# Performance work log

Hardware: AMD Instinct MI355X
Metric: run time of the kernel (lower is better)

Reference implementation:

```python
import jax, jax.numpy as jnp
import numpy as np

N = 65536
E = 1048576
IN_DIM, HID, OUT = 500, 256, 64
ALPHA = 0.1
K = 10


def setup_inputs() -> dict:
    key = jax.random.key(0)
    ks = jax.random.split(key, 12)
    x = jax.random.normal(ks[0], (N, IN_DIM), dtype=jnp.float32)
    edge_row = jax.random.randint(ks[1], (E,), 0, N, dtype=jnp.int32)
    edge_col = jax.random.randint(ks[2], (E,), 0, N, dtype=jnp.int32)
    edge_weight = jax.random.uniform(ks[3], (E,), dtype=jnp.float32)
    # Linear params (Kaiming-uniform-like scale)
    def lin(k, fan_in, fan_out):
        kw, kb = jax.random.split(k)
        bound = 1.0 / np.sqrt(fan_in)
        W = jax.random.uniform(kw, (fan_in, fan_out), minval=-bound, maxval=bound, dtype=jnp.float32)
        b = jax.random.uniform(kb, (fan_out,), minval=-bound, maxval=bound, dtype=jnp.float32)
        return W, b
    W1, b1 = lin(ks[4], IN_DIM, HID)
    W2, b2 = lin(ks[5], HID, HID)
    W3, b3 = lin(ks[6], HID, OUT)
    return {"x": x, "W1": W1, "b1": b1, "W2": W2, "b2": b2,
            "W3": W3, "b3": b3, "edge_weight": edge_weight,
            "edge_row": edge_row, "edge_col": edge_col}


def reference(x, W1, b1, W2, b2, W3, b3, edge_weight, edge_row, edge_col):
    # MLP stack (dropout=0.0, norm_type='none')
    h = jax.nn.relu(x @ W1 + b1)          # [N, HID]
    h = jax.nn.relu(h @ W2 + b2)          # [N, HID]
    h = h @ W3 + b3                        # [N, OUT]
    h0 = h
    w = edge_weight[:, None]               # [E, 1]
    # APPNP: k steps of h = (1-alpha) * (A @ h) + alpha * h0 (SpMM via segment_sum)
    def step(h, _):
        msg = h[edge_col] * w               # [E, OUT] gather + scale
        agg = jax.ops.segment_sum(msg, edge_row, num_segments=N)  # [N, OUT]
        return (1.0 - ALPHA) * agg + ALPHA * h0, None
    h, _ = jax.lax.scan(step, h, None, length=K)
    return h
```

## Files before the change

kernel.cpp:

```cpp
#include <hip/hip_runtime.h>
#include <cstdint>
#include <cstddef>


#define N_NODES   65536
#define N_EDGES   1048576
#define IN_DIM    500
#define IN_PAD    512
#define HID_DIM   256
#define OUT_DIM   64
#define K_STEPS   10

#define NPW   8
#define CAPW  608
#define NCHUNK 16

typedef _Float16 half8 __attribute__((ext_vector_type(8)));
typedef float    f32x4 __attribute__((ext_vector_type(4)));

#define XB_OFF    0ULL
#define HA_OFF    0ULL
#define HB_OFF    33554432ULL
#define H1_OFF    67108864ULL
#define H0_OFF    67108864ULL
#define H2_OFF    100663296ULL
#define CNT2_OFF  100663296ULL
#define RANK_OFF  104857600ULL
#define TOT_OFF   109051904ULL
#define W1T_OFF   134217728ULL
#define W2T_OFF   134479872ULL
#define W3T_OFF   134610944ULL
#define ROWP_OFF  134643712ULL
#define EDG_OFF   135430400ULL

__device__ __forceinline__ void gload_lds16(const void* g, void* l) {
  __builtin_amdgcn_global_load_lds(
      (const __attribute__((address_space(1))) void*)g,
      (__attribute__((address_space(3))) void*)l, 16, 0, 0);
}

__device__ __forceinline__ float bf2f(unsigned short u) {
  return __uint_as_float(((unsigned)u) << 16);
}
__device__ __forceinline__ unsigned short f2bf_rne(float f) {
  unsigned u = __float_as_uint(f);
  u += 0x7fffu + ((u >> 16) & 1u);
  return (unsigned short)(u >> 16);
}
__device__ __forceinline__ float uaf(int u) {
  return __uint_as_float((unsigned)u);
}

template <int TM, int TN, int WM, int WN, bool RELU, int OMODE>
__global__ __launch_bounds__(256)
void gemm_kernel(const _Float16* __restrict__ A, const _Float16* __restrict__ B,
                 const float* __restrict__ bias, void* __restrict__ Cout,
                 int M, int Nn, int K) {
  static_assert((TM * 8) % 256 == 0 && (TN * 8) % 256 == 0, "tile");
  __shared__ uint4 As[TM * 8];
  __shared__ uint4 Bs[TN * 8];
  const int t    = threadIdx.x;
  const int lane = t & 63;
  const int wave = t >> 6;
  const int wm   = wave / WN;
  const int wn   = wave % WN;
  const int row0 = blockIdx.x * TM;
  const int col0 = blockIdx.y * TN;
  const int l15  = lane & 15;
  const int lq   = lane >> 4;

  f32x4 acc[4][4];
#pragma unroll
  for (int i = 0; i < 4; ++i)
#pragma unroll
    for (int j = 0; j < 4; ++j) acc[i][j] = (f32x4){0.f, 0.f, 0.f, 0.f};

  for (int k0 = 0; k0 < K; k0 += 64) {
#pragma unroll
    for (int i = 0; i < (TM * 8) / 256; ++i) {
      const int c = i * 256 + wave * 64 + lane;
      const int q = c / TM;
      const int r = c % TM;
      gload_lds16(A + (size_t)(row0 + r) * K + (k0 + q * 8),
                  As + i * 256 + wave * 64);
    }
#pragma unroll
    for (int i = 0; i < (TN * 8) / 256; ++i) {
      const int c = i * 256 + wave * 64 + lane;
      const int q = c / TN;
      const int r = c % TN;
      gload_lds16(B + (size_t)(col0 + r) * K + (k0 + q * 8),
                  Bs + i * 256 + wave * 64);
    }
    __syncthreads();
#pragma unroll
    for (int kk = 0; kk < 2; ++kk) {
      const int qa = kk * 4 + lq;
      half8 af[4], bfr[4];
#pragma unroll
      for (int mt = 0; mt < 4; ++mt)
        af[mt] = *((const half8*)(As + (qa * TM + wm * 64 + mt * 16 + l15)));
#pragma unroll
      for (int nt = 0; nt < 4; ++nt)
        bfr[nt] = *((const half8*)(Bs + (qa * TN + wn * 64 + nt * 16 + l15)));
#pragma unroll
      for (int mt = 0; mt < 4; ++mt)
#pragma unroll
        for (int nt = 0; nt < 4; ++nt)
          acc[mt][nt] = __builtin_amdgcn_mfma_f32_16x16x32_f16(
              af[mt], bfr[nt], acc[mt][nt], 0, 0, 0);
    }
    __syncthreads();
  }

#pragma unroll
  for (int mt = 0; mt < 4; ++mt) {
#pragma unroll
    for (int nt = 0; nt < 4; ++nt) {
      const int col = col0 + wn * 64 + nt * 16 + l15;
      const float bv = bias[col];
#pragma unroll
      for (int r = 0; r < 4; ++r) {
        const int row = row0 + wm * 64 + mt * 16 + lq * 4 + r;
        float v = acc[mt][nt][r] + bv;
        if (RELU) v = fmaxf(v, 0.f);
        if (OMODE == 0)
          ((_Float16*)Cout)[(size_t)row * Nn + col] = (_Float16)v;
        else if (OMODE == 1)
          ((unsigned short*)Cout)[(size_t)row * Nn + col] = f2bf_rne(v);
        else
          ((float*)Cout)[(size_t)row * Nn + col] = v;
      }
    }
  }
}

__global__ void cast_x_kernel(const float* __restrict__ x,
                              _Float16* __restrict__ xb) {
  const int c = blockIdx.x * blockDim.x + threadIdx.x;
  if (c >= N_NODES * (IN_PAD / 8)) return;
  const int row = c >> 6;
  const int c8  = (c & 63) << 3;
  half8 o;
  if (c8 + 8 <= IN_DIM) {
    const float4* p = (const float4*)(x + (size_t)row * IN_DIM + c8);
    const float4 a = p[0], b = p[1];
    o[0] = (_Float16)a.x; o[1] = (_Float16)a.y;
    o[2] = (_Float16)a.z; o[3] = (_Float16)a.w;
    o[4] = (_Float16)b.x; o[5] = (_Float16)b.y;
    o[6] = (_Float16)b.z; o[7] = (_Float16)b.w;
  } else {
#pragma unroll
    for (int j = 0; j < 8; ++j) {
      const float v = (c8 + j < IN_DIM) ? x[(size_t)row * IN_DIM + c8 + j] : 0.f;
      o[j] = (_Float16)v;
    }
  }
  *(half8*)(xb + (size_t)c * 8) = o;
}

__global__ void cast_w_kernel(const float* __restrict__ W,
                              _Float16* __restrict__ Wt, int K, int Kpad,
                              int Nn) {
  const int idx = blockIdx.x * blockDim.x + threadIdx.x;
  if (idx >= Nn * Kpad) return;
  const int n = idx / Kpad;
  const int k = idx % Kpad;
  const float v = (k < K) ? W[(size_t)k * Nn + n] : 0.f;
  Wt[idx] = (_Float16)v;
}

__global__ void hist2_kernel(const int* __restrict__ row,
                             int* __restrict__ cnt2, int* __restrict__ rank,
                             int E) {
  const int e = blockIdx.x * blockDim.x + threadIdx.x;
  if (e < E)
    rank[e] = atomicAdd(&cnt2[(e >> 16) * N_NODES + row[e]], 1);
}

__global__ void scan_tot_kernel(const int* __restrict__ cnt2,
                                int* __restrict__ tot) {
  const int r = blockIdx.x * blockDim.x + threadIdx.x;
  int s = 0;
#pragma unroll
  for (int c = 0; c < NCHUNK; ++c) s += cnt2[c * N_NODES + r];
  tot[r] = s;
}

__global__ void scan_kernel(const int4* __restrict__ counts4,
                            int* __restrict__ rowptr) {
  __shared__ int part[1024];
  const int t = threadIdx.x;
  const int base = t * 16;
  int4 c[16];
  int s = 0;
#pragma unroll
  for (int i = 0; i < 16; ++i) {
    c[i] = counts4[base + i];
    s += c[i].x + c[i].y + c[i].z + c[i].w;
  }
  part[t] = s;
  __syncthreads();
  for (int off = 1; off < 1024; off <<= 1) {
    const int v = (t >= off) ? part[t - off] : 0;
    __syncthreads();
    part[t] += v;
    __syncthreads();
  }
  int run = (t == 0) ? 0 : part[t - 1];
#pragma unroll
  for (int i = 0; i < 16; ++i) {
    int4 r;
    r.x = run; run += c[i].x;
    r.y = run; run += c[i].y;
    r.z = run; run += c[i].z;
    r.w = run; run += c[i].w;
    ((int4*)rowptr)[base + i] = r;
  }
  if (t == 1023) rowptr[N_NODES] = run;
}

__global__ void chunkbase_kernel(int* __restrict__ cnt2,
                                 const int* __restrict__ rowptr) {
  const int r = blockIdx.x * blockDim.x + threadIdx.x;
  int run = rowptr[r];
#pragma unroll
  for (int c = 0; c < NCHUNK; ++c) {
    const int t = cnt2[c * N_NODES + r];
    cnt2[c * N_NODES + r] = run;
    run += t;
  }
}

__global__ void scatter2_kernel(const int* __restrict__ row,
                                const int* __restrict__ col,
                                const float* __restrict__ w,
                                const int* __restrict__ rank,
                                const int* __restrict__ cbase,
                                int2* __restrict__ edges, int E) {
  const int e = blockIdx.x * blockDim.x + threadIdx.x;
  if (e < E) {
    const int pos = cbase[(e >> 16) * N_NODES + row[e]] + rank[e];
    edges[pos] = make_int2(col[e], __float_as_int(w[e]));
  }
}

template <bool OUT_F32>
__global__ __launch_bounds__(256)
void prop_step(const unsigned short* __restrict__ hin,
               const unsigned short* __restrict__ h0,
               void* __restrict__ hout, const int* __restrict__ rowptr,
               const int2* __restrict__ edges) {
  __shared__ int2 eb[4][CAPW];
  const int wave = threadIdx.x >> 6;
  const int lane = threadIdx.x & 63;
  const int node0 = (blockIdx.x * 4 + wave) * NPW;

  const int rp  = rowptr[node0 + min(lane, NPW)];
  const int beg = __shfl(rp, 0);
  const int nE  = __shfl(rp, NPW) - beg;
  const int rrel = rp - beg;
  int2* __restrict__ ebw = eb[wave];

  const bool fast = (nE <= CAPW);
  if (fast) {
    for (int i = lane; i < nE; i += 64) ebw[i] = edges[beg + i];
    __builtin_amdgcn_s_waitcnt(0);
  }

  for (int i = 0; i < NPW; ++i) {
    const int nb = __shfl(rrel, i);
    const int ne = __shfl(rrel, i + 1);
    float a0 = 0.f, a1 = 0.f, a2 = 0.f, a3 = 0.f;
    if (fast) {
      int j = nb;
      for (; j + 8 <= ne; j += 8) {
        const int2 e0 = ebw[j + 0];
        const int2 e1 = ebw[j + 1];
        const int2 e2 = ebw[j + 2];
        const int2 e3 = ebw[j + 3];
        const int2 e4 = ebw[j + 4];
        const int2 e5 = ebw[j + 5];
        const int2 e6 = ebw[j + 6];
        const int2 e7 = ebw[j + 7];
        const float v0 = bf2f(hin[((size_t)e0.x << 6) | lane]);
        const float v1 = bf2f(hin[((size_t)e1.x << 6) | lane]);
        const float v2 = bf2f(hin[((size_t)e2.x << 6) | lane]);
        const float v3 = bf2f(hin[((size_t)e3.x << 6) | lane]);
        const float v4 = bf2f(hin[((size_t)e4.x << 6) | lane]);
        const float v5 = bf2f(hin[((size_t)e5.x << 6) | lane]);
        const float v6 = bf2f(hin[((size_t)e6.x << 6) | lane]);
        const float v7 = bf2f(hin[((size_t)e7.x << 6) | lane]);
        a0 = fmaf(uaf(e0.y), v0, a0);
        a1 = fmaf(uaf(e1.y), v1, a1);
        a2 = fmaf(uaf(e2.y), v2, a2);
        a3 = fmaf(uaf(e3.y), v3, a3);
        a0 = fmaf(uaf(e4.y), v4, a0);
        a1 = fmaf(uaf(e5.y), v5, a1);
        a2 = fmaf(uaf(e6.y), v6, a2);
        a3 = fmaf(uaf(e7.y), v7, a3);
      }
      for (; j + 4 <= ne; j += 4) {
        const int2 e0 = ebw[j + 0];
        const int2 e1 = ebw[j + 1];
        const int2 e2 = ebw[j + 2];
        const int2 e3 = ebw[j + 3];
        const float v0 = bf2f(hin[((size_t)e0.x << 6) | lane]);
        const float v1 = bf2f(hin[((size_t)e1.x << 6) | lane]);
        const float v2 = bf2f(hin[((size_t)e2.x << 6) | lane]);
        const float v3 = bf2f(hin[((size_t)e3.x << 6) | lane]);
        a0 = fmaf(uaf(e0.y), v0, a0);
        a1 = fmaf(uaf(e1.y), v1, a1);
        a2 = fmaf(uaf(e2.y), v2, a2);
        a3 = fmaf(uaf(e3.y), v3, a3);
      }
      for (; j < ne; ++j) {
        const int2 e = ebw[j];
        a0 = fmaf(uaf(e.y), bf2f(hin[((size_t)e.x << 6) | lane]), a0);
      }
    } else {
      for (int j = nb; j < ne; ++j) {
        const int2 e = edges[beg + j];
        a0 = fmaf(uaf(e.y), bf2f(hin[((size_t)e.x << 6) | lane]), a0);
      }
    }
    const float acc = (a0 + a1) + (a2 + a3);
    const size_t o = ((size_t)(node0 + i) << 6) | lane;
    const float r = 0.9f * acc + 0.1f * bf2f(h0[o]);
    if (OUT_F32)
      ((float*)hout)[o] = r;
    else
      ((unsigned short*)hout)[o] = f2bf_rne(r);
  }
}

extern "C" void kernel_launch(void* const* d_in, const int* in_sizes, int n_in,
                              void* d_out, int out_size, void* d_ws,
                              size_t ws_size, hipStream_t stream) {
  const float* x  = (const float*)d_in[0];
  const float* W1 = (const float*)d_in[1];
  const float* b1 = (const float*)d_in[2];
  const float* W2 = (const float*)d_in[3];
  const float* b2 = (const float*)d_in[4];
  const float* W3 = (const float*)d_in[5];
  const float* b3 = (const float*)d_in[6];
  const float* ew = (const float*)d_in[7];
  const int* erow = (const int*)d_in[8];
  const int* ecol = (const int*)d_in[9];

  char* ws = (char*)d_ws;
  _Float16* xb  = (_Float16*)(ws + XB_OFF);
  _Float16* h1  = (_Float16*)(ws + H1_OFF);
  _Float16* h2  = (_Float16*)(ws + H2_OFF);
  _Float16* w1t = (_Float16*)(ws + W1T_OFF);
  _Float16* w2t = (_Float16*)(ws + W2T_OFF);
  _Float16* w3t = (_Float16*)(ws + W3T_OFF);
  unsigned short* h0b = (unsigned short*)(ws + H0_OFF);
  unsigned short* hAb = (unsigned short*)(ws + HA_OFF);
  unsigned short* hBb = (unsigned short*)(ws + HB_OFF);
  int* rowp     = (int*)(ws + ROWP_OFF);
  int* cnt2     = (int*)(ws + CNT2_OFF);
  int* rankb    = (int*)(ws + RANK_OFF);
  int* tot      = (int*)(ws + TOT_OFF);
  int2* edges   = (int2*)(ws + EDG_OFF);
  float* outp   = (float*)d_out;

  hipMemsetAsync(cnt2, 0, NCHUNK * N_NODES * sizeof(int), stream);
  hist2_kernel<<<N_EDGES / 256, 256, 0, stream>>>(erow, cnt2, rankb, N_EDGES);
  scan_tot_kernel<<<N_NODES / 256, 256, 0, stream>>>(cnt2, tot);
  scan_kernel<<<1, 1024, 0, stream>>>((const int4*)tot, rowp);
  chunkbase_kernel<<<N_NODES / 256, 256, 0, stream>>>(cnt2, rowp);
  scatter2_kernel<<<N_EDGES / 256, 256, 0, stream>>>(erow, ecol, ew, rankb,
                                                     cnt2, edges, N_EDGES);

  cast_x_kernel<<<(N_NODES * (IN_PAD / 8)) / 256, 256, 0, stream>>>(x, xb);
  cast_w_kernel<<<(HID_DIM * IN_PAD) / 256, 256, 0, stream>>>(W1, w1t, IN_DIM,
                                                              IN_PAD, HID_DIM);
  cast_w_kernel<<<(HID_DIM * HID_DIM) / 256, 256, 0, stream>>>(
      W2, w2t, HID_DIM, HID_DIM, HID_DIM);
  cast_w_kernel<<<(OUT_DIM * HID_DIM) / 256, 256, 0, stream>>>(
      W3, w3t, HID_DIM, HID_DIM, OUT_DIM);

  gemm_kernel<128, 128, 2, 2, true, 0>
      <<<dim3(N_NODES / 128, HID_DIM / 128), 256, 0, stream>>>(
          xb, w1t, b1, h1, N_NODES, HID_DIM, IN_PAD);
  gemm_kernel<128, 128, 2, 2, true, 0>
      <<<dim3(N_NODES / 128, HID_DIM / 128), 256, 0, stream>>>(
          h1, w2t, b2, h2, N_NODES, HID_DIM, HID_DIM);
  gemm_kernel<256, 64, 4, 1, false, 1>
      <<<dim3(N_NODES / 256, 1), 256, 0, stream>>>(h2, w3t, b3, h0b, N_NODES,
                                                   OUT_DIM, HID_DIM);

  for (int s = 0; s < K_STEPS - 1; ++s) {
    const unsigned short* hin = (s == 0) ? h0b : ((s - 1) & 1 ? hBb : hAb);
    unsigned short* hout = (s & 1) ? hBb : hAb;
    prop_step<false><<<N_NODES / (4 * NPW), 256, 0, stream>>>(hin, h0b, hout,
                                                              rowp, edges);
  }
  prop_step<true><<<N_NODES / (4 * NPW), 256, 0, stream>>>(
      (K_STEPS - 2) & 1 ? hBb : hAb, h0b, outp, rowp, edges);
}
```

Baseline: 660.0 us.

## Fuse x cast into first GEMM and vectorize propagation gathers

Removes the separate fp32-to-fp16 cast pass over x by converting x inside a new first-layer GEMM that covers the full 256-column width per 64-row block. The second GEMM changes to a 64x256 tile shape. The propagation kernel now has each lane load two bf16 features as one 32-bit word, with the two half-waves handling alternating edges and combining through a cross-half shuffle. This cuts per-edge gather instructions and the xb round trip through memory, at the cost of an unpipelined in-kernel cast and extra shuffle work.

```diff
diff --git a/kernel.cpp b/kernel.cpp
--- a/kernel.cpp
+++ b/kernel.cpp
@@ -18,7 +18,6 @@
 typedef _Float16 half8 __attribute__((ext_vector_type(8)));
 typedef float    f32x4 __attribute__((ext_vector_type(4)));
 
-#define XB_OFF    0ULL
 #define HA_OFF    0ULL
 #define HB_OFF    33554432ULL
 #define H1_OFF    67108864ULL
@@ -49,6 +48,12 @@
 }
 __device__ __forceinline__ float uaf(int u) {
   return __uint_as_float((unsigned)u);
+}
+__device__ __forceinline__ float lo16(unsigned v) {
+  return __uint_as_float(v << 16);
+}
+__device__ __forceinline__ float hi16(unsigned v) {
+  return __uint_as_float(v & 0xffff0000u);
 }
 
 template <int TM, int TN, int WM, int WN, bool RELU, int OMODE>
@@ -135,28 +140,90 @@
   }
 }
 
-__global__ void cast_x_kernel(const float* __restrict__ x,
-                              _Float16* __restrict__ xb) {
-  const int c = blockIdx.x * blockDim.x + threadIdx.x;
-  if (c >= N_NODES * (IN_PAD / 8)) return;
-  const int row = c >> 6;
-  const int c8  = (c & 63) << 3;
-  half8 o;
-  if (c8 + 8 <= IN_DIM) {
-    const float4* p = (const float4*)(x + (size_t)row * IN_DIM + c8);
-    const float4 a = p[0], b = p[1];
-    o[0] = (_Float16)a.x; o[1] = (_Float16)a.y;
-    o[2] = (_Float16)a.z; o[3] = (_Float16)a.w;
-    o[4] = (_Float16)b.x; o[5] = (_Float16)b.y;
-    o[6] = (_Float16)b.z; o[7] = (_Float16)b.w;
-  } else {
-#pragma unroll
-    for (int j = 0; j < 8; ++j) {
-      const float v = (c8 + j < IN_DIM) ? x[(size_t)row * IN_DIM + c8 + j] : 0.f;
-      o[j] = (_Float16)v;
-    }
-  }
-  *(half8*)(xb + (size_t)c * 8) = o;
+__global__ __launch_bounds__(256)
+void gemm1_fused(const float* __restrict__ x, const _Float16* __restrict__ B,
+                 const float* __restrict__ bias, _Float16* __restrict__ C) {
+  __shared__ uint4 As[64 * 8];
+  __shared__ uint4 Bs[256 * 8];
+  const int t    = threadIdx.x;
+  const int lane = t & 63;
+  const int wave = t >> 6;
+  const int row0 = blockIdx.x * 64;
+  const int l15  = lane & 15;
+  const int lq   = lane >> 4;
+
+  f32x4 acc[4][4];
+#pragma unroll
+  for (int i = 0; i < 4; ++i)
+#pragma unroll
+    for (int j = 0; j < 4; ++j) acc[i][j] = (f32x4){0.f, 0.f, 0.f, 0.f};
+
+  for (int k0 = 0; k0 < IN_PAD; k0 += 64) {
+#pragma unroll
+    for (int i = 0; i < 2; ++i) {
+      const int c  = i * 256 + t;
+      const int q  = c >> 6;
+      const int r  = c & 63;
+      const int kb = k0 + q * 8;
+      const float* src = x + (size_t)(row0 + r) * IN_DIM + kb;
+      half8 o;
+      if (kb + 8 <= IN_DIM) {
+        const float4 a = ((const float4*)src)[0];
+        const float4 b = ((const float4*)src)[1];
+        o[0] = (_Float16)a.x; o[1] = (_Float16)a.y;
+        o[2] = (_Float16)a.z; o[3] = (_Float16)a.w;
+        o[4] = (_Float16)b.x; o[5] = (_Float16)b.y;
+        o[6] = (_Float16)b.z; o[7] = (_Float16)b.w;
+      } else {
+#pragma unroll
+        for (int jj = 0; jj < 8; ++jj)
+          o[jj] = (kb + jj < IN_DIM) ? (_Float16)src[jj] : (_Float16)0.f;
+      }
+      *(half8*)(As + c) = o;
+    }
+#pragma unroll
+    for (int i = 0; i < 8; ++i) {
+      const int c = i * 256 + wave * 64 + lane;
+      const int q = c >> 8;
+      const int r = c & 255;
+      gload_lds16(B + (size_t)r * IN_PAD + (k0 + q * 8),
+                  Bs + i * 256 + wave * 64);
+    }
+    __syncthreads();
+#pragma unroll
+    for (int kk = 0; kk < 2; ++kk) {
+      const int qa = kk * 4 + lq;
+      half8 af[4], bfr[4];
+#pragma unroll
+      for (int mt = 0; mt < 4; ++mt)
+        af[mt] = *((const half8*)(As + (qa * 64 + mt * 16 + l15)));
+#pragma unroll
+      for (int nt = 0; nt < 4; ++nt)
+        bfr[nt] = *((const half8*)(Bs + (qa * 256 + wave * 64 + nt * 16 + l15)));
+#pragma unroll
+      for (int mt = 0; mt < 4; ++mt)
+#pragma unroll
+        for (int nt = 0; nt < 4; ++nt)
+          acc[mt][nt] = __builtin_amdgcn_mfma_f32_16x16x32_f16(
+              af[mt], bfr[nt], acc[mt][nt], 0, 0, 0);
+    }
+    __syncthreads();
+  }
+
+#pragma unroll
+  for (int mt = 0; mt < 4; ++mt) {
+#pragma unroll
+    for (int nt = 0; nt < 4; ++nt) {
+      const int col = wave * 64 + nt * 16 + l15;
+      const float bv = bias[col];
+#pragma unroll
+      for (int r = 0; r < 4; ++r) {
+        const int row = row0 + mt * 16 + lq * 4 + r;
+        const float v = fmaxf(acc[mt][nt][r] + bv, 0.f);
+        C[(size_t)row * HID_DIM + col] = (_Float16)v;
+      }
+    }
+  }
 }
 
 __global__ void cast_w_kernel(const float* __restrict__ W,
@@ -254,7 +321,11 @@
   __shared__ int2 eb[4][CAPW];
   const int wave = threadIdx.x >> 6;
   const int lane = threadIdx.x & 63;
+  const int half = lane >> 5;
+  const int lp   = lane & 31;
   const int node0 = (blockIdx.x * 4 + wave) * NPW;
+  const unsigned* __restrict__ hin32 = (const unsigned*)hin;
+  const unsigned* __restrict__ h032  = (const unsigned*)h0;
 
   const int rp  = rowptr[node0 + min(lane, NPW)];
   const int beg = __shfl(rp, 0);
@@ -271,66 +342,62 @@
   for (int i = 0; i < NPW; ++i) {
     const int nb = __shfl(rrel, i);
     const int ne = __shfl(rrel, i + 1);
-    float a0 = 0.f, a1 = 0.f, a2 = 0.f, a3 = 0.f;
+    float ax0 = 0.f, ay0 = 0.f, ax1 = 0.f, ay1 = 0.f;
+    int j = nb;
     if (fast) {
-      int j = nb;
       for (; j + 8 <= ne; j += 8) {
-        const int2 e0 = ebw[j + 0];
-        const int2 e1 = ebw[j + 1];
-        const int2 e2 = ebw[j + 2];
-        const int2 e3 = ebw[j + 3];
-        const int2 e4 = ebw[j + 4];
-        const int2 e5 = ebw[j + 5];
-        const int2 e6 = ebw[j + 6];
-        const int2 e7 = ebw[j + 7];
-        const float v0 = bf2f(hin[((size_t)e0.x << 6) | lane]);
-        const float v1 = bf2f(hin[((size_t)e1.x << 6) | lane]);
-        const float v2 = bf2f(hin[((size_t)e2.x << 6) | lane]);
-        const float v3 = bf2f(hin[((size_t)e3.x << 6) | lane]);
-        const float v4 = bf2f(hin[((size_t)e4.x << 6) | lane]);
-        const float v5 = bf2f(hin[((size_t)e5.x << 6) | lane]);
-        const float v6 = bf2f(hin[((size_t)e6.x << 6) | lane]);
-        const float v7 = bf2f(hin[((size_t)e7.x << 6) | lane]);
-        a0 = fmaf(uaf(e0.y), v0, a0);
-        a1 = fmaf(uaf(e1.y), v1, a1);
-        a2 = fmaf(uaf(e2.y), v2, a2);
-        a3 = fmaf(uaf(e3.y), v3, a3);
-        a0 = fmaf(uaf(e4.y), v4, a0);
-        a1 = fmaf(uaf(e5.y), v5, a1);
-        a2 = fmaf(uaf(e6.y), v6, a2);
-        a3 = fmaf(uaf(e7.y), v7, a3);
-      }
-      for (; j + 4 <= ne; j += 4) {
-        const int2 e0 = ebw[j + 0];
-        const int2 e1 = ebw[j + 1];
-        const int2 e2 = ebw[j + 2];
-        const int2 e3 = ebw[j + 3];
-        const float v0 = bf2f(hin[((size_t)e0.x << 6) | lane]);
-        const float v1 = bf2f(hin[((size_t)e1.x << 6) | lane]);
-        const float v2 = bf2f(hin[((size_t)e2.x << 6) | lane]);
-        const float v3 = bf2f(hin[((size_t)e3.x << 6) | lane]);
-        a0 = fmaf(uaf(e0.y), v0, a0);
-        a1 = fmaf(uaf(e1.y), v1, a1);
-        a2 = fmaf(uaf(e2.y), v2, a2);
-        a3 = fmaf(uaf(e3.y), v3, a3);
-      }
-      for (; j < ne; ++j) {
+        const int2 e0 = ebw[j + 0 + half];
+        const int2 e1 = ebw[j + 2 + half];
+        const int2 e2 = ebw[j + 4 + half];
+        const int2 e3 = ebw[j + 6 + half];
+        const unsigned v0 = hin32[(e0.x << 5) | lp];
+        const unsigned v1 = hin32[(e1.x << 5) | lp];
+        const unsigned v2 = hin32[(e2.x << 5) | lp];
+        const unsigned v3 = hin32[(e3.x << 5) | lp];
+        const float w0 = uaf(e0.y), w1 = uaf(e1.y);
+        const float w2 = uaf(e2.y), w3 = uaf(e3.y);
+        ax0 = fmaf(w0, lo16(v0), ax0); ay0 = fmaf(w0, hi16(v0), ay0);
+        ax1 = fmaf(w1, lo16(v1), ax1); ay1 = fmaf(w1, hi16(v1), ay1);
+        ax0 = fmaf(w2, lo16(v2), ax0); ay0 = fmaf(w2, hi16(v2), ay0);
+        ax1 = fmaf(w3, lo16(v3), ax1); ay1 = fmaf(w3, hi16(v3), ay1);
+      }
+      for (; j + 2 <= ne; j += 2) {
+        const int2 e = ebw[j + half];
+        const unsigned v = hin32[(e.x << 5) | lp];
+        const float w = uaf(e.y);
+        ax0 = fmaf(w, lo16(v), ax0); ay0 = fmaf(w, hi16(v), ay0);
+      }
+      if (j < ne) {
         const int2 e = ebw[j];
-        a0 = fmaf(uaf(e.y), bf2f(hin[((size_t)e.x << 6) | lane]), a0);
+        const unsigned v = hin32[(e.x << 5) | lp];
+        const float w = half ? 0.f : uaf(e.y);
+        ax0 = fmaf(w, lo16(v), ax0); ay0 = fmaf(w, hi16(v), ay0);
       }
     } else {
-      for (int j = nb; j < ne; ++j) {
-        const int2 e = edges[beg + j];
-        a0 = fmaf(uaf(e.y), bf2f(hin[((size_t)e.x << 6) | lane]), a0);
-      }
-    }
-    const float acc = (a0 + a1) + (a2 + a3);
-    const size_t o = ((size_t)(node0 + i) << 6) | lane;
-    const float r = 0.9f * acc + 0.1f * bf2f(h0[o]);
-    if (OUT_F32)
-      ((float*)hout)[o] = r;
-    else
-      ((unsigned short*)hout)[o] = f2bf_rne(r);
+      for (; j < ne; j += 2) {
+        const int idx = j + half;
+        const int2 e = edges[beg + (idx < ne ? idx : ne - 1)];
+        const float w = (idx < ne) ? uaf(e.y) : 0.f;
+        const unsigned v = hin32[(e.x << 5) | lp];
+        ax0 = fmaf(w, lo16(v), ax0); ay0 = fmaf(w, hi16(v), ay0);
+      }
+    }
+    float sx = ax0 + ax1;
+    float sy = ay0 + ay1;
+    sx += __shfl_xor(sx, 32);
+    sy += __shfl_xor(sy, 32);
+    const int o32 = ((node0 + i) << 5) | lp;
+    const unsigned h0v = h032[o32];
+    const float r0 = 0.9f * sx + 0.1f * lo16(h0v);
+    const float r1 = 0.9f * sy + 0.1f * hi16(h0v);
+    if (half == 0) {
+      if (OUT_F32) {
+        ((float2*)hout)[o32] = make_float2(r0, r1);
+      } else {
+        ((unsigned*)hout)[o32] =
+            (unsigned)f2bf_rne(r0) | ((unsigned)f2bf_rne(r1) << 16);
+      }
+    }
   }
 }
 
@@ -349,7 +416,6 @@
   const int* ecol = (const int*)d_in[9];
 
   char* ws = (char*)d_ws;
-  _Float16* xb  = (_Float16*)(ws + XB_OFF);
   _Float16* h1  = (_Float16*)(ws + H1_OFF);
   _Float16* h2  = (_Float16*)(ws + H2_OFF);
   _Float16* w1t = (_Float16*)(ws + W1T_OFF);
@@ -373,7 +439,6 @@
   scatter2_kernel<<<N_EDGES / 256, 256, 0, stream>>>(erow, ecol, ew, rankb,
                                                      cnt2, edges, N_EDGES);
 
-  cast_x_kernel<<<(N_NODES * (IN_PAD / 8)) / 256, 256, 0, stream>>>(x, xb);
   cast_w_kernel<<<(HID_DIM * IN_PAD) / 256, 256, 0, stream>>>(W1, w1t, IN_DIM,
                                                               IN_PAD, HID_DIM);
   cast_w_kernel<<<(HID_DIM * HID_DIM) / 256, 256, 0, stream>>>(
@@ -381,12 +446,10 @@
   cast_w_kernel<<<(OUT_DIM * HID_DIM) / 256, 256, 0, stream>>>(
       W3, w3t, HID_DIM, HID_DIM, OUT_DIM);
 
-  gemm_kernel<128, 128, 2, 2, true, 0>
-      <<<dim3(N_NODES / 128, HID_DIM / 128), 256, 0, stream>>>(
-          xb, w1t, b1, h1, N_NODES, HID_DIM, IN_PAD);
-  gemm_kernel<128, 128, 2, 2, true, 0>
-      <<<dim3(N_NODES / 128, HID_DIM / 128), 256, 0, stream>>>(
-          h1, w2t, b2, h2, N_NODES, HID_DIM, HID_DIM);
+  gemm1_fused<<<dim3(N_NODES / 64), 256, 0, stream>>>(x, w1t, b1, h1);
+  gemm_kernel<64, 256, 1, 4, true, 0>
+      <<<dim3(N_NODES / 64, 1), 256, 0, stream>>>(h1, w2t, b2, h2, N_NODES,
+                                                  HID_DIM, HID_DIM);
   gemm_kernel<256, 64, 4, 1, false, 1>
       <<<dim3(N_NODES / 256, 1), 256, 0, stream>>>(h2, w3t, b3, h0b, N_NODES,
                                                    OUT_DIM, HID_DIM);
```

Result: no change. 651.4 us (-1.3%).

## Split propagation features into two 32-column halves with packed bf16 pair loads

Applied to the files above, without the earlier changes.

The GEMM epilogue now writes h0 in a column-split layout with two planes of 32 bf16 features per node. Each propagation step runs as two launches, one per half, so each gathered working set is half the size and fits better in cache. Within a wave, four 16-lane groups each handle a different edge and load packed bf16 pairs as 32-bit words, then reduce across groups with shuffles. This doubles launches and re-reads the edge list twice per step, and three-quarters of lanes sit idle during the output write.

```diff
diff --git a/kernel.cpp b/kernel.cpp
--- a/kernel.cpp
+++ b/kernel.cpp
@@ -33,15 +33,14 @@
 #define ROWP_OFF  134643712ULL
 #define EDG_OFF   135430400ULL
 
+#define HALF_U32  ((size_t)N_NODES * 16)
+
 __device__ __forceinline__ void gload_lds16(const void* g, void* l) {
   __builtin_amdgcn_global_load_lds(
       (const __attribute__((address_space(1))) void*)g,
       (__attribute__((address_space(3))) void*)l, 16, 0, 0);
 }
 
-__device__ __forceinline__ float bf2f(unsigned short u) {
-  return __uint_as_float(((unsigned)u) << 16);
-}
 __device__ __forceinline__ unsigned short f2bf_rne(float f) {
   unsigned u = __float_as_uint(f);
   u += 0x7fffu + ((u >> 16) & 1u);
@@ -49,6 +48,12 @@
 }
 __device__ __forceinline__ float uaf(int u) {
   return __uint_as_float((unsigned)u);
+}
+__device__ __forceinline__ float lo16(unsigned v) {
+  return __uint_as_float(v << 16);
+}
+__device__ __forceinline__ float hi16(unsigned v) {
+  return __uint_as_float(v & 0xffff0000u);
 }
 
 template <int TM, int TN, int WM, int WN, bool RELU, int OMODE>
@@ -128,8 +133,11 @@
           ((_Float16*)Cout)[(size_t)row * Nn + col] = (_Float16)v;
         else if (OMODE == 1)
           ((unsigned short*)Cout)[(size_t)row * Nn + col] = f2bf_rne(v);
+        else if (OMODE == 2)
+          ((float*)Cout)[(size_t)row * Nn + col] = v;
         else
-          ((float*)Cout)[(size_t)row * Nn + col] = v;
+          ((unsigned short*)Cout)[(size_t)(col >> 5) * ((size_t)N_NODES * 32) +
+                                  (size_t)row * 32 + (col & 31)] = f2bf_rne(v);
       }
     }
   }
@@ -247,13 +255,16 @@
 
 template <bool OUT_F32>
 __global__ __launch_bounds__(256)
-void prop_step(const unsigned short* __restrict__ hin,
-               const unsigned short* __restrict__ h0,
-               void* __restrict__ hout, const int* __restrict__ rowptr,
+void prop_half(const unsigned* __restrict__ hin,
+               const unsigned* __restrict__ h0,
+               void* __restrict__ hout,
+               const int* __restrict__ rowptr,
                const int2* __restrict__ edges) {
   __shared__ int2 eb[4][CAPW];
   const int wave = threadIdx.x >> 6;
   const int lane = threadIdx.x & 63;
+  const int grp  = lane >> 4;
+  const int lg   = lane & 15;
   const int node0 = (blockIdx.x * 4 + wave) * NPW;
 
   const int rp  = rowptr[node0 + min(lane, NPW)];
@@ -271,66 +282,65 @@
   for (int i = 0; i < NPW; ++i) {
     const int nb = __shfl(rrel, i);
     const int ne = __shfl(rrel, i + 1);
-    float a0 = 0.f, a1 = 0.f, a2 = 0.f, a3 = 0.f;
+    float ax0 = 0.f, ay0 = 0.f, ax1 = 0.f, ay1 = 0.f;
+    int j = nb;
     if (fast) {
-      int j = nb;
-      for (; j + 8 <= ne; j += 8) {
-        const int2 e0 = ebw[j + 0];
-        const int2 e1 = ebw[j + 1];
-        const int2 e2 = ebw[j + 2];
-        const int2 e3 = ebw[j + 3];
-        const int2 e4 = ebw[j + 4];
-        const int2 e5 = ebw[j + 5];
-        const int2 e6 = ebw[j + 6];
-        const int2 e7 = ebw[j + 7];
-        const float v0 = bf2f(hin[((size_t)e0.x << 6) | lane]);
-        const float v1 = bf2f(hin[((size_t)e1.x << 6) | lane]);
-        const float v2 = bf2f(hin[((size_t)e2.x << 6) | lane]);
-        const float v3 = bf2f(hin[((size_t)e3.x << 6) | lane]);
-        const float v4 = bf2f(hin[((size_t)e4.x << 6) | lane]);
-        const float v5 = bf2f(hin[((size_t)e5.x << 6) | lane]);
-        const float v6 = bf2f(hin[((size_t)e6.x << 6) | lane]);
-        const float v7 = bf2f(hin[((size_t)e7.x << 6) | lane]);
-        a0 = fmaf(uaf(e0.y), v0, a0);
-        a1 = fmaf(uaf(e1.y), v1, a1);
-        a2 = fmaf(uaf(e2.y), v2, a2);
-        a3 = fmaf(uaf(e3.y), v3, a3);
-        a0 = fmaf(uaf(e4.y), v4, a0);
-        a1 = fmaf(uaf(e5.y), v5, a1);
-        a2 = fmaf(uaf(e6.y), v6, a2);
-        a3 = fmaf(uaf(e7.y), v7, a3);
+      for (; j + 16 <= ne; j += 16) {
+        const int2 e0 = ebw[j + grp];
+        const int2 e1 = ebw[j + 4 + grp];
+        const int2 e2 = ebw[j + 8 + grp];
+        const int2 e3 = ebw[j + 12 + grp];
+        const unsigned v0 = hin[(e0.x << 4) | lg];
+        const unsigned v1 = hin[(e1.x << 4) | lg];
+        const unsigned v2 = hin[(e2.x << 4) | lg];
+        const unsigned v3 = hin[(e3.x << 4) | lg];
+        const float w0 = uaf(e0.y), w1 = uaf(e1.y);
+        const float w2 = uaf(e2.y), w3 = uaf(e3.y);
+        ax0 = fmaf(w0, lo16(v0), ax0); ay0 = fmaf(w0, hi16(v0), ay0);
+        ax1 = fmaf(w1, lo16(v1), ax1); ay1 = fmaf(w1, hi16(v1), ay1);
+        ax0 = fmaf(w2, lo16(v2), ax0); ay0 = fmaf(w2, hi16(v2), ay0);
+        ax1 = fmaf(w3, lo16(v3), ax1); ay1 = fmaf(w3, hi16(v3), ay1);
       }
       for (; j + 4 <= ne; j += 4) {
-        const int2 e0 = ebw[j + 0];
-        const int2 e1 = ebw[j + 1];
-        const int2 e2 = ebw[j + 2];
-        const int2 e3 = ebw[j + 3];
-        const float v0 = bf2f(hin[((size_t)e0.x << 6) | lane]);
-        const float v1 = bf2f(hin[((size_t)e1.x << 6) | lane]);
-        const float v2 = bf2f(hin[((size_t)e2.x << 6) | lane]);
-        const float v3 = bf2f(hin[((size_t)e3.x << 6) | lane]);
-        a0 = fmaf(uaf(e0.y), v0, a0);
-        a1 = fmaf(uaf(e1.y), v1, a1);
-        a2 = fmaf(uaf(e2.y), v2, a2);
-        a3 = fmaf(uaf(e3.y), v3, a3);
-      }
-      for (; j < ne; ++j) {
-        const int2 e = ebw[j];
-        a0 = fmaf(uaf(e.y), bf2f(hin[((size_t)e.x << 6) | lane]), a0);
+        const int2 e = ebw[j + grp];
+        const unsigned v = hin[(e.x << 4) | lg];
+        const float w = uaf(e.y);
+        ax0 = fmaf(w, lo16(v), ax0); ay0 = fmaf(w, hi16(v), ay0);
+      }
+      if (j < ne) {
+        const int idx = j + grp;
+        const int2 e = ebw[idx < ne ? idx : ne - 1];
+        const float w = (idx < ne) ? uaf(e.y) : 0.f;
+        const unsigned v = hin[(e.x << 4) | lg];
+        ax0 = fmaf(w, lo16(v), ax0); ay0 = fmaf(w, hi16(v), ay0);
       }
     } else {
-      for (int j = nb; j < ne; ++j) {
-        const int2 e = edges[beg + j];
-        a0 = fmaf(uaf(e.y), bf2f(hin[((size_t)e.x << 6) | lane]), a0);
-      }
-    }
-    const float acc = (a0 + a1) + (a2 + a3);
-    const size_t o = ((size_t)(node0 + i) << 6) | lane;
-    const float r = 0.9f * acc + 0.1f * bf2f(h0[o]);
-    if (OUT_F32)
-      ((float*)hout)[o] = r;
-    else
-      ((unsigned short*)hout)[o] = f2bf_rne(r);
+      for (; j < ne; j += 4) {
+        const int idx = j + grp;
+        const int2 e = edges[beg + (idx < ne ? idx : ne - 1)];
+        const float w = (idx < ne) ? uaf(e.y) : 0.f;
+        const unsigned v = hin[(e.x << 4) | lg];
+        ax0 = fmaf(w, lo16(v), ax0); ay0 = fmaf(w, hi16(v), ay0);
+      }
+    }
+    float sx = ax0 + ax1;
+    float sy = ay0 + ay1;
+    sx += __shfl_xor(sx, 16); sx += __shfl_xor(sx, 32);
+    sy += __shfl_xor(sy, 16); sy += __shfl_xor(sy, 32);
+    const int node = node0 + i;
+    const int o = (node << 4) | lg;
+    const unsigned h0v = h0[o];
+    const float r0 = 0.9f * sx + 0.1f * lo16(h0v);
+    const float r1 = 0.9f * sy + 0.1f * hi16(h0v);
+    if (grp == 0) {
+      if (OUT_F32) {
+        ((float2*)((float*)hout + ((size_t)node << 6)))[lg] =
+            make_float2(r0, r1);
+      } else {
+        ((unsigned*)hout)[o] =
+            (unsigned)f2bf_rne(r0) | ((unsigned)f2bf_rne(r1) << 16);
+      }
+    }
   }
 }
 
@@ -355,9 +365,9 @@
   _Float16* w1t = (_Float16*)(ws + W1T_OFF);
   _Float16* w2t = (_Float16*)(ws + W2T_OFF);
   _Float16* w3t = (_Float16*)(ws + W3T_OFF);
-  unsigned short* h0b = (unsigned short*)(ws + H0_OFF);
-  unsigned short* hAb = (unsigned short*)(ws + HA_OFF);
-  unsigned short* hBb = (unsigned short*)(ws + HB_OFF);
+  unsigned* h0h = (unsigned*)(ws + H0_OFF);
+  unsigned* hAh = (unsigned*)(ws + HA_OFF);
+  unsigned* hBh = (unsigned*)(ws + HB_OFF);
   int* rowp     = (int*)(ws + ROWP_OFF);
   int* cnt2     = (int*)(ws + CNT2_OFF);
   int* rankb    = (int*)(ws + RANK_OFF);
@@ -387,16 +397,23 @@
   gemm_kernel<128, 128, 2, 2, true, 0>
       <<<dim3(N_NODES / 128, HID_DIM / 128), 256, 0, stream>>>(
           h1, w2t, b2, h2, N_NODES, HID_DIM, HID_DIM);
-  gemm_kernel<256, 64, 4, 1, false, 1>
-      <<<dim3(N_NODES / 256, 1), 256, 0, stream>>>(h2, w3t, b3, h0b, N_NODES,
+  gemm_kernel<256, 64, 4, 1, false, 3>
+      <<<dim3(N_NODES / 256, 1), 256, 0, stream>>>(h2, w3t, b3, h0h, N_NODES,
                                                    OUT_DIM, HID_DIM);
 
-  for (int s = 0; s < K_STEPS - 1; ++s) {
-    const unsigned short* hin = (s == 0) ? h0b : ((s - 1) & 1 ? hBb : hAb);
-    unsigned short* hout = (s & 1) ? hBb : hAb;
-    prop_step<false><<<N_NODES / (4 * NPW), 256, 0, stream>>>(hin, h0b, hout,
-                                                              rowp, edges);
-  }
-  prop_step<true><<<N_NODES / (4 * NPW), 256, 0, stream>>>(
-      (K_STEPS - 2) & 1 ? hBb : hAb, h0b, outp, rowp, edges);
-}
+  for (int s = 0; s < K_STEPS; ++s) {
+    const bool last = (s == K_STEPS - 1);
+    const unsigned* hin = (s == 0) ? h0h : ((s - 1) & 1 ? hBh : hAh);
+    unsigned* hout = (s & 1) ? hBh : hAh;
+    for (int half = 0; half < 2; ++half) {
+      const unsigned* hinH = hin + half * HALF_U32;
+      const unsigned* h0H  = h0h + half * HALF_U32;
+      if (!last)
+        prop_half<false><<<N_NODES / (4 * NPW), 256, 0, stream>>>(
+            hinH, h0H, hout + half * HALF_U32, rowp, edges);
+      else
+        prop_half<true><<<N_NODES / (4 * NPW), 256, 0, stream>>>(
+            hinH, h0H, outp + half * 32, rowp, edges);
+    }
+  }
+}
```

New measurement: 782.6 us. +18.6%, slower.
